# Optimization experiments

Hardware: AMD Instinct MI355X
Metric: run time of the kernel (lower is better)

Reference implementation:

```python
import jax, jax.numpy as jnp
import numpy as np

N_NODES = 50000
N_EDGES = 800000
NUM_FEATURES = 3
HIDDEN = 128
NUM_GRAPHS = 100
NUM_CLASSES = 2


def setup_inputs() -> dict:
    key = jax.random.key(0)
    ks = jax.random.split(key, 12)
    x = jax.random.normal(ks[0], (N_NODES, NUM_FEATURES), dtype=jnp.float32)
    edge_index = jax.random.randint(ks[1], (2, N_EDGES), 0, N_NODES, dtype=jnp.int64)
    batch = jnp.sort(jax.random.randint(ks[2], (N_NODES,), 0, NUM_GRAPHS, dtype=jnp.int64))
    c1, c2, c3 = 4 * HIDDEN, 2 * HIDDEN, HIDDEN  # 512, 256, 128

    def glorot(k, fan_in, fan_out):
        s = jnp.sqrt(6.0 / (fan_in + fan_out)).astype(jnp.float32)
        return jax.random.uniform(k, (fan_in, fan_out), jnp.float32, -s, s)

    W1 = glorot(ks[3], NUM_FEATURES, c1); b1 = jnp.zeros((c1,), jnp.float32)
    W2 = glorot(ks[4], c1, c2);           b2 = jnp.zeros((c2,), jnp.float32)
    W3 = glorot(ks[5], c2, c3);           b3 = jnp.zeros((c3,), jnp.float32)
    Wc = glorot(ks[6], c3, NUM_CLASSES);  bc = jnp.zeros((NUM_CLASSES,), jnp.float32)
    return {"x": x, "W1": W1, "b1": b1, "W2": W2, "b2": b2, "W3": W3, "b3": b3,
            "Wc": Wc, "bc": bc, "edge_index": edge_index, "batch": batch}


def reference(x, W1, b1, W2, b2, W3, b3, Wc, bc, edge_index, batch):
    n = x.shape[0]
    self_loop = jnp.arange(n, dtype=edge_index.dtype)
    row = jnp.concatenate([edge_index[0], self_loop])  # source nodes (messages from)
    col = jnp.concatenate([edge_index[1], self_loop])  # target nodes (aggregate into)
    # symmetric GCN normalization with self-loops: deg^{-1/2}[row] * deg^{-1/2}[col]
    deg = jax.ops.segment_sum(jnp.ones(row.shape, x.dtype), col, num_segments=n)
    dis = jnp.where(deg > 0, jax.lax.rsqrt(jnp.maximum(deg, 1.0)), 0.0)
    norm = dis[row] * dis[col]  # [E + N]

    def gcn_conv(h, W, b):
        m = h @ W                                   # project first (cheap GEMM)
        agg = jax.ops.segment_sum(norm[:, None] * m[row], col, num_segments=n)
        return agg + b

    h = jax.nn.relu(gcn_conv(x, W1, b1))
    h = jax.nn.relu(gcn_conv(h, W2, b2))
    h = jax.nn.relu(gcn_conv(h, W3, b3))

    # global mean pool over graphs
    counts = jax.ops.segment_sum(jnp.ones((n,), h.dtype), batch, num_segments=NUM_GRAPHS)
    pooled = jax.ops.segment_sum(h, batch, num_segments=NUM_GRAPHS) / jnp.maximum(counts, 1.0)[:, None]

    logits = pooled @ Wc + bc
    return jax.nn.log_softmax(logits, axis=1)
```

## Files before the change

kernel.cpp:

```cpp
#include <hip/hip_runtime.h>
#include <hip/hip_bf16.h>
#include <hip/hip_fp8.h>
#include <math.h>

#define N_NODES 50000
#define N_EDGES 800000
#define NFEAT 3
#define C1 512
#define C2 256
#define C3 128
#define NGRAPH 100
#define NCLS 2
#define PSPLIT 8
#define NRANGE 8
#define RANGE_SZ 6250
#define NE4 200000
#define NRCHUNK 391
#define WBLK 640

typedef short bh8 __attribute__((ext_vector_type(8)));
typedef float f32x4 __attribute__((ext_vector_type(4)));

__device__ __forceinline__ short f2bf(float x) {
    __hip_bfloat16 h = __float2bfloat16(x);
    return *reinterpret_cast<short*>(&h);
}
__device__ __forceinline__ float bflo(unsigned int u) { return __uint_as_float(u << 16); }
__device__ __forceinline__ float bfhi(unsigned int u) { return __uint_as_float(u & 0xffff0000u); }
__device__ __forceinline__ unsigned int packbf(float a, float b) {
    return (unsigned int)(unsigned short)f2bf(a) | ((unsigned int)(unsigned short)f2bf(b) << 16);
}
__device__ __forceinline__ unsigned char f2fp8(float x) {
    __hip_fp8_e4m3 q(x);
    return (unsigned char)q.__x;
}
__device__ __forceinline__ float2 fp8x2(unsigned short u) {
    __hip_fp8x2_e4m3 q; q.__x = u; return (float2)q;
}

__device__ __forceinline__ void gload16(const void* g, void* l) {
    __builtin_amdgcn_global_load_lds((const __attribute__((address_space(1))) void*)g,
                                     (__attribute__((address_space(3))) void*)l, 16, 0, 0);
}


__global__ void count_prep(const int4* __restrict__ col4, int* __restrict__ counts,
                           const float* __restrict__ W2, const float* __restrict__ W3,
                           short* __restrict__ W2t, short* __restrict__ W3t) {
    int b = blockIdx.x;
    if (b < NRCHUNK * NRANGE) {
        int range = b & (NRANGE - 1);
        int lo = range * RANGE_SZ, hi = lo + RANGE_SZ;
        int base = (b >> 3) * 512 + threadIdx.x;
#pragma unroll
        for (int h = 0; h < 2; ++h) {
            int i = base + h * 256;
            if (i < NE4) {
                int4 c = col4[i];
                if (c.x >= lo && c.x < hi) atomicAdd(&counts[c.x], 1);
                if (c.y >= lo && c.y < hi) atomicAdd(&counts[c.y], 1);
                if (c.z >= lo && c.z < hi) atomicAdd(&counts[c.z], 1);
                if (c.w >= lo && c.w < hi) atomicAdd(&counts[c.w], 1);
            }
        }
    } else {
        int idx = (b - NRCHUNK * NRANGE) * 256 + threadIdx.x;
        if (idx < C1 * C2) {
            int n = idx / C1, k = idx % C1;
            W2t[idx] = f2bf(W2[k * C2 + n]);
        } else if (idx < C1 * C2 + C2 * C3) {
            int j = idx - C1 * C2;
            int n = j / C2, k = j % C2;
            W3t[j] = f2bf(W3[k * C3 + n]);
        }
    }
}


__global__ void scan_chunks(const int* __restrict__ counts, const float* __restrict__ x,
                            int* __restrict__ offsets, int* __restrict__ chunksums,
                            float* __restrict__ dis, float4* __restrict__ xd) {
    __shared__ int s[256];
    int b = blockIdx.x, t = threadIdx.x;
    int i = b * 256 + t;
    int v = (i < N_NODES) ? counts[i] : 0;
    if (i < N_NODES) {
        float d = rsqrtf((float)(v + 1));
        dis[i] = d;
        xd[i] = make_float4(x[i * 3 + 0], x[i * 3 + 1], x[i * 3 + 2], d);
    }
    s[t] = v;
    __syncthreads();
    for (int d = 1; d < 256; d <<= 1) {
        int add = (t >= d) ? s[t - d] : 0;
        __syncthreads();
        s[t] += add;
        __syncthreads();
    }
    if (i < N_NODES) offsets[i + 1] = s[t];
    if (t == 255) chunksums[b] = s[255];
}


__global__ void finalize_offsets(int* __restrict__ offsets, const int* __restrict__ chunksums,
                                 int* __restrict__ cursor) {
    __shared__ int s[256];
    int b = blockIdx.x, t = threadIdx.x;
    int nck = (N_NODES + 255) / 256;
    s[t] = (t < nck) ? chunksums[t] : 0;
    __syncthreads();
    for (int d = 1; d < 256; d <<= 1) {
        int add = (t >= d) ? s[t - d] : 0;
        __syncthreads();
        s[t] += add;
        __syncthreads();
    }
    int add = (b == 0) ? 0 : s[b - 1];
    int i = b * 256 + t;
    if (i < N_NODES) {
        int val = offsets[i + 1] + add;
        offsets[i + 1] = val;
        if (i + 1 < N_NODES) cursor[i + 1] = val;
    }
    if (i == 0) { offsets[0] = 0; cursor[0] = 0; }
}


__global__ void scatter_edges(const int4* __restrict__ row4, const int4* __restrict__ col4,
                              int* __restrict__ cursor, int* __restrict__ csr_src) {
    int b = blockIdx.x;
    int range = b & (NRANGE - 1);
    int lo = range * RANGE_SZ, hi = lo + RANGE_SZ;
    int base = (b >> 3) * 512 + threadIdx.x;
#pragma unroll
    for (int h = 0; h < 2; ++h) {
        int i = base + h * 256;
        if (i < NE4) {
            int4 c = col4[i];
            int4 r = row4[i];
            if (c.x >= lo && c.x < hi) { int p = atomicAdd(&cursor[c.x], 1); csr_src[p] = r.x; }
            if (c.y >= lo && c.y < hi) { int p = atomicAdd(&cursor[c.y], 1); csr_src[p] = r.y; }
            if (c.z >= lo && c.z < hi) { int p = atomicAdd(&cursor[c.z], 1); csr_src[p] = r.z; }
            if (c.w >= lo && c.w < hi) { int p = atomicAdd(&cursor[c.w], 1); csr_src[p] = r.w; }
        }
    }
}


__global__ __launch_bounds__(512, 4) void gemm_l1(const float4* __restrict__ xd,
                                                  const int* __restrict__ offsets,
                                                  const int* __restrict__ csr_src,
                                                  const float* __restrict__ W1,
                                                  const float* __restrict__ b1,
                                                  const short* __restrict__ Bt,
                                                  unsigned char* __restrict__ Cmat, int M) {
    __shared__ short As[128 * 32];
    __shared__ short Bs[C2 * 32];
    __shared__ float sW1[3 * C1];
    __shared__ float sb1[C1];
    __shared__ float sa[128 * 3];
    __shared__ float sd[128];
    int bm = blockIdx.x * 128;
    int t = threadIdx.x;
    int wave = t >> 6, lane = t & 63, quad = lane >> 4, l16 = lane & 15;
    int wm = (wave >> 2) * 64;
    int wn = (wave & 3) * 64;
    f32x4 acc[4][4] = {};

    for (int j = t; j < 3 * C1; j += 512) sW1[j] = W1[j];
    if (t < C1) sb1[t] = b1[t];

    int lg = t & 15;
#pragma unroll
    for (int rnd = 0; rnd < 4; ++rnd) {
        int rloc = rnd * 32 + (t >> 4);
        int i = bm + rloc; if (i > M - 1) i = M - 1;
        int s0 = offsets[i], e0 = offsets[i + 1];
        float a0 = 0.f, a1 = 0.f, a2 = 0.f;
        for (int p = s0 + lg; p < e0; p += 16) {
            int r = csr_src[p];
            float4 v = xd[r];
            a0 += v.w * v.x;
            a1 += v.w * v.y;
            a2 += v.w * v.z;
        }
#pragma unroll
        for (int m = 1; m < 16; m <<= 1) {
            a0 += __shfl_xor(a0, m);
            a1 += __shfl_xor(a1, m);
            a2 += __shfl_xor(a2, m);
        }
        if (lg == 0) {
            float4 self = xd[i];
            float di = self.w;
            a0 += di * self.x; a1 += di * self.y; a2 += di * self.z;
            sa[rloc * 3 + 0] = di * a0;
            sa[rloc * 3 + 1] = di * a1;
            sa[rloc * 3 + 2] = di * a2;
            sd[rloc] = di;
        }
    }
    __syncthreads();

    int ar = t >> 2, ak = (t & 3) * 8;
    float a0 = sa[ar * 3 + 0], a1 = sa[ar * 3 + 1], a2 = sa[ar * 3 + 2];
    float drow = sd[ar];

    int c0 = t, c1 = 512 + t;
    int b0row = c0 >> 2, b0off = (c0 & 3) * 8;
    int b1row = c1 >> 2, b1off = (c1 & 3) * 8;

    for (int k0 = 0; k0 < C1; k0 += 32) {
#pragma unroll
        for (int j = 0; j < 8; ++j) {
            int k = k0 + ak + j;
            float v = a0 * sW1[k] + a1 * sW1[C1 + k] + a2 * sW1[2 * C1 + k] + sb1[k];
            As[ar * 32 + ak + j] = f2bf(drow * fmaxf(v, 0.f));
        }
        gload16(Bt + (size_t)b0row * C1 + k0 + b0off, &Bs[c0 * 8]);
        gload16(Bt + (size_t)b1row * C1 + k0 + b1off, &Bs[c1 * 8]);
        __syncthreads();
        bh8 af[4], bf[4];
#pragma unroll
        for (int mt = 0; mt < 4; ++mt)
            af[mt] = *(const bh8*)&As[(wm + mt * 16 + l16) * 32 + quad * 8];
#pragma unroll
        for (int nt = 0; nt < 4; ++nt)
            bf[nt] = *(const bh8*)&Bs[(wn + nt * 16 + l16) * 32 + quad * 8];
#pragma unroll
        for (int mt = 0; mt < 4; ++mt)
#pragma unroll
            for (int nt = 0; nt < 4; ++nt)
                acc[mt][nt] = __builtin_amdgcn_mfma_f32_16x16x32_bf16(af[mt], bf[nt], acc[mt][nt], 0, 0, 0);
        __syncthreads();
    }

#pragma unroll
    for (int mt = 0; mt < 4; ++mt)
#pragma unroll
        for (int nt = 0; nt < 4; ++nt) {
            int colc = wn + nt * 16 + l16;
#pragma unroll
            for (int r = 0; r < 4; ++r) {
                int rowc = bm + wm + mt * 16 + quad * 4 + r;
                if (rowc < M) Cmat[(size_t)rowc * C2 + colc] = f2fp8(acc[mt][nt][r]);
            }
        }
}


template <int K, int BN>
__global__ __launch_bounds__(512, 4) void gemm_bf16(const short* __restrict__ A,
                                                    const short* __restrict__ Bt,
                                                    unsigned char* __restrict__ Cmat, int M) {
    __shared__ short As[128 * 32];
    __shared__ short Bs[BN * 32];
    constexpr int NT = BN / 64;
    int bm = blockIdx.x * 128;
    int t = threadIdx.x;
    int wave = t >> 6, lane = t & 63, quad = lane >> 4, l16 = lane & 15;
    int wm = (wave >> 2) * 64;
    int wn = (wave & 3) * (BN / 4);
    f32x4 acc[4][NT] = {};

    int ar = t >> 2, ak = (t & 3) * 8;
    int agr = bm + ar; if (agr > M - 1) agr = M - 1;
    const short* aptr = A + (size_t)agr * K + ak;
    const short* bptr = Bt + (size_t)(t >> 2) * K + ((t & 3) * 8);

    for (int k0 = 0; k0 < K; k0 += 32) {
        gload16(aptr + k0, &As[t * 8]);
        static_assert(BN == 128, "staging specialized for BN==128");
        gload16(bptr + k0, &Bs[t * 8]);
        __syncthreads();
        bh8 af[4], bf[NT];
#pragma unroll
        for (int mt = 0; mt < 4; ++mt)
            af[mt] = *(const bh8*)&As[(wm + mt * 16 + l16) * 32 + quad * 8];
#pragma unroll
        for (int nt = 0; nt < NT; ++nt)
            bf[nt] = *(const bh8*)&Bs[(wn + nt * 16 + l16) * 32 + quad * 8];
#pragma unroll
        for (int mt = 0; mt < 4; ++mt)
#pragma unroll
            for (int nt = 0; nt < NT; ++nt)
                acc[mt][nt] = __builtin_amdgcn_mfma_f32_16x16x32_bf16(af[mt], bf[nt], acc[mt][nt], 0, 0, 0);
        __syncthreads();
    }

#pragma unroll
    for (int mt = 0; mt < 4; ++mt)
#pragma unroll
        for (int nt = 0; nt < NT; ++nt) {
            int colc = wn + nt * 16 + l16;
#pragma unroll
            for (int r = 0; r < 4; ++r) {
                int rowc = bm + wm + mt * 16 + quad * 4 + r;
                if (rowc < M) Cmat[(size_t)rowc * BN + colc] = f2fp8(acc[mt][nt][r]);
            }
        }
}


template <int C, bool PRESCALE>
__global__ __launch_bounds__(256) void aggregate_w(const unsigned char* __restrict__ m,
                                                   const int* __restrict__ offsets,
                                                   const int* __restrict__ csr_src,
                                                   const float* __restrict__ dis,
                                                   const float* __restrict__ bias,
                                                   short* __restrict__ out) {
    int i = blockIdx.x * 4 + (threadIdx.x >> 6);
    if (i >= N_NODES) return;
    int lane = threadIdx.x & 63;
    int s = __builtin_amdgcn_readfirstlane(offsets[i]);
    int e = __builtin_amdgcn_readfirstlane(offsets[i + 1]);
    float di = __uint_as_float(__builtin_amdgcn_readfirstlane(__float_as_uint(dis[i])));

    if constexpr (C == 256) {
        const unsigned int* mu = (const unsigned int*)m;
        unsigned int su = mu[(size_t)i * (C / 4) + lane];
        float2 slo = fp8x2((unsigned short)(su & 0xffffu));
        float2 shi = fp8x2((unsigned short)(su >> 16));
        float a0 = slo.x, a1 = slo.y, a2 = shi.x, a3 = shi.y;
        int p = s;
        for (; p + 16 <= e; p += 16) {
            unsigned int u[16];
#pragma unroll
            for (int j = 0; j < 16; ++j) {
                int r = csr_src[p + j];
                u[j] = mu[(size_t)r * (C / 4) + lane];
            }
#pragma unroll
            for (int j = 0; j < 16; ++j) {
                float2 lo = fp8x2((unsigned short)(u[j] & 0xffffu));
                float2 hi = fp8x2((unsigned short)(u[j] >> 16));
                a0 += lo.x; a1 += lo.y; a2 += hi.x; a3 += hi.y;
            }
        }
        if (p < e) {
            unsigned int u[16];
            float sc[16];
#pragma unroll
            for (int j = 0; j < 16; ++j) {
                int q = p + j;
                sc[j] = (q < e) ? 1.f : 0.f;
                int r = csr_src[(q < e) ? q : e - 1];
                u[j] = mu[(size_t)r * (C / 4) + lane];
            }
#pragma unroll
            for (int j = 0; j < 16; ++j) {
                float2 lo = fp8x2((unsigned short)(u[j] & 0xffffu));
                float2 hi = fp8x2((unsigned short)(u[j] >> 16));
                a0 = fmaf(sc[j], lo.x, a0);
                a1 = fmaf(sc[j], lo.y, a1);
                a2 = fmaf(sc[j], hi.x, a2);
                a3 = fmaf(sc[j], hi.y, a3);
            }
        }
        float4 b = *(const float4*)&bias[4 * lane];
        a0 = fmaxf(di * a0 + b.x, 0.f);
        a1 = fmaxf(di * a1 + b.y, 0.f);
        a2 = fmaxf(di * a2 + b.z, 0.f);
        a3 = fmaxf(di * a3 + b.w, 0.f);
        if (PRESCALE) { a0 *= di; a1 *= di; a2 *= di; a3 *= di; }
        uint2 o;
        o.x = packbf(a0, a1);
        o.y = packbf(a2, a3);
        *(uint2*)(out + (size_t)i * C + 4 * lane) = o;
    } else {
        const unsigned short* mu = (const unsigned short*)m;
        float2 sf = fp8x2(mu[(size_t)i * (C / 2) + lane]);
        float a0 = sf.x, a1 = sf.y;
        int p = s;
        for (; p + 16 <= e; p += 16) {
            unsigned short u[16];
#pragma unroll
            for (int j = 0; j < 16; ++j) {
                int r = csr_src[p + j];
                u[j] = mu[(size_t)r * (C / 2) + lane];
            }
#pragma unroll
            for (int j = 0; j < 16; ++j) {
                float2 f = fp8x2(u[j]);
                a0 += f.x; a1 += f.y;
            }
        }
        if (p < e) {
            unsigned short u[16];
            float sc[16];
#pragma unroll
            for (int j = 0; j < 16; ++j) {
                int q = p + j;
                sc[j] = (q < e) ? 1.f : 0.f;
                int r = csr_src[(q < e) ? q : e - 1];
                u[j] = mu[(size_t)r * (C / 2) + lane];
            }
#pragma unroll
            for (int j = 0; j < 16; ++j) {
                float2 f = fp8x2(u[j]);
                a0 = fmaf(sc[j], f.x, a0);
                a1 = fmaf(sc[j], f.y, a1);
            }
        }
        float2 b = *(const float2*)&bias[2 * lane];
        a0 = fmaxf(di * a0 + b.x, 0.f);
        a1 = fmaxf(di * a1 + b.y, 0.f);
        if (PRESCALE) { a0 *= di; a1 *= di; }
        ((unsigned int*)out)[(size_t)i * (C / 2) + lane] = packbf(a0, a1);
    }
}


__global__ void pool_partial(const short* __restrict__ h3, const int* __restrict__ batch,
                             float* __restrict__ pooled) {
    int g = blockIdx.x, sp = blockIdx.y;
    int t = threadIdx.x;
    __shared__ int seg[2];
    if (t < 2) {
        int target = g + t;
        int lo = 0, hi = N_NODES;
        while (lo < hi) { int mid = (lo + hi) >> 1; if (batch[mid] < target) lo = mid + 1; else hi = mid; }
        seg[t] = lo;
    }
    __syncthreads();
    int start = seg[0], end = seg[1];
    int len = end - start;
    int chunk = (len + PSPLIT - 1) / PSPLIT;
    int a = start + sp * chunk;
    int b = a + chunk; if (b > end) b = end;
    if (a >= b) return;
    const unsigned int* hu = (const unsigned int*)h3;
    float s0 = 0.f, s1 = 0.f;
    int i = a;
    for (; i + 4 <= b; i += 4) {
        unsigned int u0 = hu[(size_t)(i + 0) * (C3 / 2) + t];
        unsigned int u1 = hu[(size_t)(i + 1) * (C3 / 2) + t];
        unsigned int u2 = hu[(size_t)(i + 2) * (C3 / 2) + t];
        unsigned int u3 = hu[(size_t)(i + 3) * (C3 / 2) + t];
        s0 += bflo(u0) + bflo(u1) + bflo(u2) + bflo(u3);
        s1 += bfhi(u0) + bfhi(u1) + bfhi(u2) + bfhi(u3);
    }
    for (; i < b; ++i) {
        unsigned int u = hu[(size_t)i * (C3 / 2) + t];
        s0 += bflo(u);
        s1 += bfhi(u);
    }
    atomicAdd(&pooled[g * C3 + 2 * t], s0);
    atomicAdd(&pooled[g * C3 + 2 * t + 1], s1);
}


__global__ void finalize_head(const float* __restrict__ pooled, const int* __restrict__ batch,
                              const float* __restrict__ Wc, const float* __restrict__ bc,
                              float* __restrict__ outp) {
    int g = blockIdx.x;
    int t = threadIdx.x;
    __shared__ int seg[2];
    if (t < 2) {
        int target = g + t;
        int lo = 0, hi = N_NODES;
        while (lo < hi) { int mid = (lo + hi) >> 1; if (batch[mid] < target) lo = mid + 1; else hi = mid; }
        seg[t] = lo;
    }
    __syncthreads();
    float cnt = (float)(seg[1] - seg[0]);
    float pv = pooled[(size_t)g * C3 + t] / fmaxf(cnt, 1.f);
    float p0 = pv * Wc[t * 2 + 0];
    float p1 = pv * Wc[t * 2 + 1];
#pragma unroll
    for (int o = 32; o > 0; o >>= 1) {
        p0 += __shfl_down(p0, o);
        p1 += __shfl_down(p1, o);
    }
    __shared__ float r0[2], r1[2];
    int wid = t >> 6, lane = t & 63;
    if (lane == 0) { r0[wid] = p0; r1[wid] = p1; }
    __syncthreads();
    if (t == 0) {
        float l0 = r0[0] + r0[1] + bc[0];
        float l1 = r1[0] + r1[1] + bc[1];
        float mx = fmaxf(l0, l1);
        float lse = mx + logf(expf(l0 - mx) + expf(l1 - mx));
        outp[g * 2 + 0] = l0 - lse;
        outp[g * 2 + 1] = l1 - lse;
    }
}


extern "C" void kernel_launch(void* const* d_in, const int* in_sizes, int n_in,
                              void* d_out, int out_size, void* d_ws, size_t ws_size,
                              hipStream_t stream) {
    const float* x = (const float*)d_in[0];
    const float* W1 = (const float*)d_in[1];
    const float* b1 = (const float*)d_in[2];
    const float* W2 = (const float*)d_in[3];
    const float* b2 = (const float*)d_in[4];
    const float* W3 = (const float*)d_in[5];
    const float* b3 = (const float*)d_in[6];
    const float* Wc = (const float*)d_in[7];
    const float* bc = (const float*)d_in[8];
    const int* ei = (const int*)d_in[9];
    const int* batch = (const int*)d_in[10];
    const int4* row4 = (const int4*)ei;
    const int4* col4 = (const int4*)(ei + N_EDGES);
    float* out = (float*)d_out;

    char* ws = (char*)d_ws;
    size_t off = 0;
    auto alloc = [&](size_t bytes) -> void* {
        off = (off + 255) & ~(size_t)255;
        void* p = ws + off;
        off += bytes;
        return p;
    };

    int* counts = (int*)alloc((size_t)N_NODES * 4);
    float* pooled = (float*)alloc((size_t)NGRAPH * C3 * 4);
    size_t zero_bytes = off;

    int* offsets = (int*)alloc((size_t)(N_NODES + 1) * 4);
    int* cursor = (int*)alloc((size_t)N_NODES * 4);
    int* chunksums = (int*)alloc(256 * 4);
    float* dis = (float*)alloc((size_t)N_NODES * 4);
    float4* xd = (float4*)alloc((size_t)N_NODES * 16);
    int* csr_src = (int*)alloc((size_t)N_EDGES * 4);
    short* W2t = (short*)alloc((size_t)C1 * C2 * 2);
    short* W3t = (short*)alloc((size_t)C2 * C3 * 2);
    unsigned char* m2 = (unsigned char*)alloc((size_t)N_NODES * C2);
    short* h2 = (short*)alloc((size_t)N_NODES * C2 * 2);
    unsigned char* m3 = (unsigned char*)alloc((size_t)N_NODES * C3);
    short* h3 = (short*)alloc((size_t)N_NODES * C3 * 2);

    hipMemsetAsync(ws, 0, zero_bytes, stream);

    count_prep<<<NRCHUNK * NRANGE + WBLK, 256, 0, stream>>>(col4, counts, W2, W3, W2t, W3t);
    int nchunks = (N_NODES + 255) / 256;
    scan_chunks<<<nchunks, 256, 0, stream>>>(counts, x, offsets, chunksums, dis, xd);
    finalize_offsets<<<nchunks, 256, 0, stream>>>(offsets, chunksums, cursor);
    scatter_edges<<<NRCHUNK * NRANGE, 256, 0, stream>>>(row4, col4, cursor, csr_src);

    gemm_l1<<<(N_NODES + 127) / 128, 512, 0, stream>>>(xd, offsets, csr_src, W1, b1, W2t, m2, N_NODES);
    aggregate_w<C2, true><<<(N_NODES + 3) / 4, 256, 0, stream>>>(m2, offsets, csr_src, dis, b2, h2);

    gemm_bf16<C2, C3><<<(N_NODES + 127) / 128, 512, 0, stream>>>(h2, W3t, m3, N_NODES);
    aggregate_w<C3, false><<<(N_NODES + 3) / 4, 256, 0, stream>>>(m3, offsets, csr_src, dis, b3, h3);

    dim3 gp(NGRAPH, PSPLIT);
    pool_partial<<<gp, C3 / 2, 0, stream>>>(h3, batch, pooled);
    finalize_head<<<NGRAPH, C3, 0, stream>>>(pooled, batch, Wc, bc, out);
}
```

Baseline: 279.1 us.

## Fuse mean-pool and classifier head into one block-per-graph kernel

Replaces the split pool_partial kernel (with global atomics into a zeroed pooled buffer) and the separate finalize_head kernel with a single 512-thread kernel per graph. Eight wavefronts stride over the graph's nodes, reduce through shared memory, then compute logits and log-softmax in the same block. This removes one kernel launch, the global atomics and the pooled buffer, in exchange for only 100 blocks doing the pooling reads with less parallelism than the 800 blocks used before.

```diff
diff --git a/kernel.cpp b/kernel.cpp
--- a/kernel.cpp
+++ b/kernel.cpp
@@ -11,7 +11,6 @@
 #define C3 128
 #define NGRAPH 100
 #define NCLS 2
-#define PSPLIT 8
 #define NRANGE 8
 #define RANGE_SZ 6250
 #define NE4 200000
@@ -411,11 +410,17 @@
 }
 
 
-__global__ void pool_partial(const short* __restrict__ h3, const int* __restrict__ batch,
-                             float* __restrict__ pooled) {
-    int g = blockIdx.x, sp = blockIdx.y;
+__global__ __launch_bounds__(512) void pool_head(const short* __restrict__ h3,
+                                                 const int* __restrict__ batch,
+                                                 const float* __restrict__ Wc,
+                                                 const float* __restrict__ bc,
+                                                 float* __restrict__ outp) {
+    __shared__ int seg[2];
+    __shared__ float part[8][C3];
+    __shared__ float r0[2], r1[2];
+    int g = blockIdx.x;
     int t = threadIdx.x;
-    __shared__ int seg[2];
+    int w = t >> 6, lane = t & 63;
     if (t < 2) {
         int target = g + t;
         int lo = 0, hi = N_NODES;
@@ -424,57 +429,40 @@
     }
     __syncthreads();
     int start = seg[0], end = seg[1];
-    int len = end - start;
-    int chunk = (len + PSPLIT - 1) / PSPLIT;
-    int a = start + sp * chunk;
-    int b = a + chunk; if (b > end) b = end;
-    if (a >= b) return;
     const unsigned int* hu = (const unsigned int*)h3;
     float s0 = 0.f, s1 = 0.f;
-    int i = a;
-    for (; i + 4 <= b; i += 4) {
-        unsigned int u0 = hu[(size_t)(i + 0) * (C3 / 2) + t];
-        unsigned int u1 = hu[(size_t)(i + 1) * (C3 / 2) + t];
-        unsigned int u2 = hu[(size_t)(i + 2) * (C3 / 2) + t];
-        unsigned int u3 = hu[(size_t)(i + 3) * (C3 / 2) + t];
+    int i = start + w;
+    for (; i + 24 < end; i += 32) {
+        unsigned int u0 = hu[(size_t)(i + 0)  * (C3 / 2) + lane];
+        unsigned int u1 = hu[(size_t)(i + 8)  * (C3 / 2) + lane];
+        unsigned int u2 = hu[(size_t)(i + 16) * (C3 / 2) + lane];
+        unsigned int u3 = hu[(size_t)(i + 24) * (C3 / 2) + lane];
         s0 += bflo(u0) + bflo(u1) + bflo(u2) + bflo(u3);
         s1 += bfhi(u0) + bfhi(u1) + bfhi(u2) + bfhi(u3);
     }
-    for (; i < b; ++i) {
-        unsigned int u = hu[(size_t)i * (C3 / 2) + t];
+    for (; i < end; i += 8) {
+        unsigned int u = hu[(size_t)i * (C3 / 2) + lane];
         s0 += bflo(u);
         s1 += bfhi(u);
     }
-    atomicAdd(&pooled[g * C3 + 2 * t], s0);
-    atomicAdd(&pooled[g * C3 + 2 * t + 1], s1);
-}
-
-
-__global__ void finalize_head(const float* __restrict__ pooled, const int* __restrict__ batch,
-                              const float* __restrict__ Wc, const float* __restrict__ bc,
-                              float* __restrict__ outp) {
-    int g = blockIdx.x;
-    int t = threadIdx.x;
-    __shared__ int seg[2];
-    if (t < 2) {
-        int target = g + t;
-        int lo = 0, hi = N_NODES;
-        while (lo < hi) { int mid = (lo + hi) >> 1; if (batch[mid] < target) lo = mid + 1; else hi = mid; }
-        seg[t] = lo;
-    }
+    part[w][2 * lane] = s0;
+    part[w][2 * lane + 1] = s1;
     __syncthreads();
-    float cnt = (float)(seg[1] - seg[0]);
-    float pv = pooled[(size_t)g * C3 + t] / fmaxf(cnt, 1.f);
-    float p0 = pv * Wc[t * 2 + 0];
-    float p1 = pv * Wc[t * 2 + 1];
-#pragma unroll
-    for (int o = 32; o > 0; o >>= 1) {
-        p0 += __shfl_down(p0, o);
-        p1 += __shfl_down(p1, o);
-    }
-    __shared__ float r0[2], r1[2];
-    int wid = t >> 6, lane = t & 63;
-    if (lane == 0) { r0[wid] = p0; r1[wid] = p1; }
+    if (t < C3) {
+        float v = 0.f;
+#pragma unroll
+        for (int j = 0; j < 8; ++j) v += part[j][t];
+        float cnt = fmaxf((float)(end - start), 1.f);
+        float pv = v / cnt;
+        float p0 = pv * Wc[t * 2 + 0];
+        float p1 = pv * Wc[t * 2 + 1];
+#pragma unroll
+        for (int o = 32; o > 0; o >>= 1) {
+            p0 += __shfl_down(p0, o);
+            p1 += __shfl_down(p1, o);
+        }
+        if (lane == 0) { r0[w] = p0; r1[w] = p1; }
+    }
     __syncthreads();
     if (t == 0) {
         float l0 = r0[0] + r0[1] + bc[0];
@@ -515,7 +503,6 @@
     };
 
     int* counts = (int*)alloc((size_t)N_NODES * 4);
-    float* pooled = (float*)alloc((size_t)NGRAPH * C3 * 4);
     size_t zero_bytes = off;
 
     int* offsets = (int*)alloc((size_t)(N_NODES + 1) * 4);
@@ -545,7 +532,5 @@
     gemm_bf16<C2, C3><<<(N_NODES + 127) / 128, 512, 0, stream>>>(h2, W3t, m3, N_NODES);
     aggregate_w<C3, false><<<(N_NODES + 3) / 4, 256, 0, stream>>>(m3, offsets, csr_src, dis, b3, h3);
 
-    dim3 gp(NGRAPH, PSPLIT);
-    pool_partial<<<gp, C3 / 2, 0, stream>>>(h3, batch, pooled);
-    finalize_head<<<NGRAPH, C3, 0, stream>>>(pooled, batch, Wc, bc, out);
-}
+    pool_head<<<NGRAPH, 512, 0, stream>>>(h3, batch, Wc, bc, out);
+}
```

After: 274.6 us (median of 2 runs). No clear change (-1.6%).
